# Kernel tuning notes

Hardware: AMD Instinct MI355X
Metric: run time of the kernel (lower is better)

The kernel has to match this reference:

```python
import jax, jax.numpy as jnp
import numpy as np

N_MELS = 20
NUM_FRAMES = 32
FRAME_LEN = 512
SR = NUM_FRAMES * FRAME_LEN  # 16384
EPS = np.finfo(np.float64).eps  # matches np.finfo(float).eps in original


def _mel_filters(n_fft, sr, n_mels, fmin, fmax):
    """Replicates librosa.filters.mel(..., htk=False, norm=None) in pure numpy."""
    f_sp = 200.0 / 3.0
    min_log_hz = 1000.0
    min_log_mel = min_log_hz / f_sp
    logstep = np.log(6.4) / 27.0

    def hz_to_mel(f):
        f = np.asarray(f, dtype=np.float64)
        return np.where(f >= min_log_hz,
                        min_log_mel + np.log(np.maximum(f, 1e-10) / min_log_hz) / logstep,
                        f / f_sp)

    def mel_to_hz(m):
        m = np.asarray(m, dtype=np.float64)
        return np.where(m >= min_log_mel,
                        min_log_hz * np.exp(logstep * (m - min_log_mel)),
                        f_sp * m)

    fftfreqs = np.linspace(0.0, sr / 2.0, 1 + n_fft // 2)
    mels = np.linspace(hz_to_mel(fmin), hz_to_mel(fmax), n_mels + 2)
    mel_f = mel_to_hz(mels)
    fdiff = np.diff(mel_f)
    ramps = mel_f[:, None] - fftfreqs[None, :]
    lower = -ramps[:-2] / fdiff[:-1, None]
    upper = ramps[2:] / fdiff[1:, None]
    weights = np.maximum(0.0, np.minimum(lower, upper))  # norm=None -> no scaling
    return weights.astype(np.float32)  # (n_mels, 1+n_fft//2)


def setup_inputs() -> dict:
    key = jax.random.key(0)
    inputs = jax.random.normal(key, (4096, NUM_FRAMES, FRAME_LEN), dtype=jnp.float32)
    filter_banks = jnp.asarray(_mel_filters(FRAME_LEN, SR, N_MELS, 0.0, SR / 2.0 + 1.0))
    hw = jnp.asarray(np.hamming(FRAME_LEN).astype(np.float32))
    return {"inputs": inputs, "filter_banks": filter_banks, "hw": hw}


def reference(inputs, filter_banks, hw):
    # Hamming window + forward-normalized rFFT; original squares only the REAL part.
    fft_real = jnp.fft.rfft(inputs * hw, norm="forward").real  # (B, 32, 257)
    mag = fft_real * fft_real
    mels = jnp.einsum("mf,btf->btm", filter_banks, mag)  # (B, 32, 20)
    mels = jnp.where(mels == 0, jnp.float32(EPS), mels)
    log_mels = jnp.log2(mels)
    return jnp.floor(log_mels)[..., None]  # (B, 32, 20, 1)
```

## Files before the change

kernel.cpp:

```cpp
#include <hip/hip_runtime.h>
#include <math.h>


#define MARGIN_L2 1.0e-3f
#define IDX(e) ((e) + ((e) >> 3))
#define WCSTRIDE 20

__device__ __forceinline__ float4 f4add(float4 a, float4 b) {
    return make_float4(a.x + b.x, a.y + b.y, a.z + b.z, a.w + b.w);
}
__device__ __forceinline__ float4 f4sub(float4 a, float4 b) {
    return make_float4(a.x - b.x, a.y - b.y, a.z - b.z, a.w - b.w);
}
__device__ __forceinline__ float4 cmulc4(float2 w, float4 z) {
    return make_float4(w.x * z.x + w.y * z.y, w.x * z.y - w.y * z.x,
                       w.x * z.z + w.y * z.w, w.x * z.w - w.y * z.z);
}

__device__ __forceinline__ void bfly4(int s, int l, float2 w1, float2 w2,
                                      float4 x1, float4 y1, float4 x2, float4 y2,
                                      float4* dst) {
    const int j = l >> s;
    const int r = l & ((1 << s) - 1);
    const float4 u1 = f4add(x1, y1);
    const float4 v1 = cmulc4(w1, f4sub(x1, y1));
    const float4 u2 = f4add(x2, y2);
    const float4 m  = cmulc4(w1, f4sub(x2, y2));
    const float4 v2 = make_float4(m.y, -m.x, m.w, -m.z);
    const float4 o0 = f4add(u1, u2);
    const float4 o1 = cmulc4(w2, f4sub(u1, u2));
    const float4 o2 = f4add(v1, v2);
    const float4 o3 = cmulc4(w2, f4sub(v1, v2));
    const int eb = (j << (s + 2)) + r;
    dst[IDX(eb)]            = o0;
    dst[IDX(eb + (1 << s))] = o2;
    dst[IDX(eb + (2 << s))] = o1;
    dst[IDX(eb + (3 << s))] = o3;
}

__device__ __forceinline__ void load_stage0(
    const float* __restrict__ x, int f0, int f1, int l,
    float2 h0, float2 h1, float2 h2, float2 h3,
    float2 w1, float2 w2, float4* W)
{
    const float2* xa = (const float2*)(x + (size_t)f0 * 512);
    const float2* xb = (const float2*)(x + (size_t)f1 * 512);
    const float2 a0 = xa[l],       a1 = xa[l + 64];
    const float2 a2 = xa[l + 128], a3 = xa[l + 192];
    const float2 b0 = xb[l],       b1 = xb[l + 64];
    const float2 b2 = xb[l + 128], b3 = xb[l + 192];
    const float4 x1 = make_float4(a0.x * h0.x, a0.y * h0.y,
                                  b0.x * h0.x, b0.y * h0.y);
    const float4 x2 = make_float4(a1.x * h1.x, a1.y * h1.y,
                                  b1.x * h1.x, b1.y * h1.y);
    const float4 y1 = make_float4(a2.x * h2.x, a2.y * h2.y,
                                  b2.x * h2.x, b2.y * h2.y);
    const float4 y2 = make_float4(a3.x * h3.x, a3.y * h3.y,
                                  b3.x * h3.x, b3.y * h3.y);
    bfly4(0, l, w1, w2, x1, y1, x2, y2, W);
}

__global__ void prep_full(const float* __restrict__ fb,
                          double* __restrict__ tw64,
                          float4* __restrict__ twp,
                          float4* __restrict__ wc,
                          int*    __restrict__ meta,
                          unsigned* count) {
    __shared__ float2 s_tw[256];
    __shared__ int sg0[20], sng[20];
    const int t = threadIdx.x;
    double s, c;
    sincospi((double)t * (1.0 / 256.0), &s, &c);
    tw64[t]       = c;
    tw64[256 + t] = s;
    s_tw[t] = make_float2((float)c, (float)s);

    if (t < 20) {
        int lo = 257, hi = 0;
        for (int k = 0; k < 257; k++) {
            if (fb[t * 257 + k] > 0.0f) {
                if (k < lo) lo = k;
                hi = k + 1;
            }
        }
        if (hi <= lo) { lo = 0; hi = 1; }
        int g0 = lo >> 2;
        int ng = ((hi + 3) >> 2) - g0;
        if (ng > WCSTRIDE) ng = WCSTRIDE;
        sg0[t] = g0; sng[t] = ng;
        meta[t] = g0 | (ng << 16);
    }
    __syncthreads();

    if (t < 64) {
        const float2 a0 = s_tw[2 * t],        b0 = s_tw[4 * t];
        twp[t]        = make_float4(a0.x, a0.y, b0.x, b0.y);
        const float2 a2 = s_tw[8 * (t >> 2)], b2 = s_tw[16 * (t >> 2)];
        twp[64 + t]   = make_float4(a2.x, a2.y, b2.x, b2.y);
        const float2 a4 = s_tw[32 * (t >> 4)], b4 = s_tw[64 * (t >> 4)];
        twp[128 + t]  = make_float4(a4.x, a4.y, b4.x, b4.y);
        const float2 u0 = s_tw[t],            u1 = s_tw[t + 64];
        twp[192 + t]  = make_float4(u0.x, u0.y, u1.x, u1.y);
    }

    for (int i = t; i < 20 * WCSTRIDE; i += 256) {
        const int m = i / WCSTRIDE, j = i % WCSTRIDE;
        float4 v = make_float4(0.0f, 0.0f, 0.0f, 0.0f);
        if (j < sng[m]) {
            const int b = (sg0[m] + j) * 4;
            const float* row = fb + m * 257;
            v.x = (b + 0 < 257) ? row[b + 0] : 0.0f;
            v.y = (b + 1 < 257) ? row[b + 1] : 0.0f;
            v.z = (b + 2 < 257) ? row[b + 2] : 0.0f;
            v.w = (b + 3 < 257) ? row[b + 3] : 0.0f;
        }
        wc[i] = v;
    }
    if (count && t == 0) *count = 0;
}

__global__ void prep_tw64(double* __restrict__ tw64) {
    const int t = threadIdx.x;
    double s, c;
    sincospi((double)t * (1.0 / 256.0), &s, &c);
    tw64[t]       = c;
    tw64[256 + t] = s;
}

__global__ __launch_bounds__(256, 4) void phase1(
    const float* __restrict__ x,
    const float* __restrict__ hw,
    const float4* __restrict__ twp,
    const float4* __restrict__ wc,
    const int*    __restrict__ meta,
    float* __restrict__ out,
    unsigned* __restrict__ count,
    unsigned* __restrict__ worklist)
{
    __shared__ __align__(16) float4 buf[8][288];

    const int t = threadIdx.x;
    const int w = t >> 6;
    const int l = t & 63;
    const int base = (blockIdx.x * 4 + w) * 4;
    const int fg0 = base, fg1 = base + 1, fg2 = base + 2, fg3 = base + 3;

    const float4 tp0 = twp[l];
    const float4 tp2 = twp[64 + l];
    const float4 tp4 = twp[128 + l];
    const float4 tpU = twp[192 + l];
    const float2 w0s = make_float2(tp0.x, tp0.y), w0d = make_float2(tp0.z, tp0.w);
    const float2 w2s = make_float2(tp2.x, tp2.y), w2d = make_float2(tp2.z, tp2.w);
    const float2 w4s = make_float2(tp4.x, tp4.y), w4d = make_float2(tp4.z, tp4.w);

    float4* const WA = &buf[2 * w][0];
    float4* const WB = &buf[2 * w + 1][0];

    const float2* hp = (const float2*)hw;
    const float2 h0 = hp[l],       h1 = hp[l + 64];
    const float2 h2 = hp[l + 128], h3 = hp[l + 192];

    load_stage0(x, fg0, fg1, l, h0, h1, h2, h3, w0s, w0d, WA);
    load_stage0(x, fg2, fg3, l, h0, h1, h2, h3, w0s, w0d, WB);
    __builtin_amdgcn_wave_barrier();

    {
        const float4 ax1 = WA[IDX(l)],      ay1 = WA[IDX(l + 128)];
        const float4 ax2 = WA[IDX(l + 64)], ay2 = WA[IDX(l + 192)];
        const float4 bx1 = WB[IDX(l)],      by1 = WB[IDX(l + 128)];
        const float4 bx2 = WB[IDX(l + 64)], by2 = WB[IDX(l + 192)];
        bfly4(2, l, w2s, w2d, ax1, ay1, ax2, ay2, WA);
        bfly4(2, l, w2s, w2d, bx1, by1, bx2, by2, WB);
        __builtin_amdgcn_wave_barrier();
    }
    {
        const float4 ax1 = WA[IDX(l)],      ay1 = WA[IDX(l + 128)];
        const float4 ax2 = WA[IDX(l + 64)], ay2 = WA[IDX(l + 192)];
        const float4 bx1 = WB[IDX(l)],      by1 = WB[IDX(l + 128)];
        const float4 bx2 = WB[IDX(l + 64)], by2 = WB[IDX(l + 192)];
        bfly4(4, l, w4s, w4d, ax1, ay1, ax2, ay2, WA);
        bfly4(4, l, w4s, w4d, bx1, by1, bx2, by2, WB);
        __builtin_amdgcn_wave_barrier();
    }
    {
        const float4 ax1 = WA[IDX(l)],      ay1 = WA[IDX(l + 128)];
        const float4 ax2 = WA[IDX(l + 64)], ay2 = WA[IDX(l + 192)];
        const float4 bx1 = WB[IDX(l)],      by1 = WB[IDX(l + 128)];
        const float4 bx2 = WB[IDX(l + 64)], by2 = WB[IDX(l + 192)];
        {
            const float4 u1 = f4add(ax1, ay1);
            const float4 v1 = f4sub(ax1, ay1);
            const float4 u2 = f4add(ax2, ay2);
            const float4 m  = f4sub(ax2, ay2);
            const float4 v2 = make_float4(m.y, -m.x, m.w, -m.z);
            WA[IDX(l)]       = f4add(u1, u2);
            WA[IDX(l + 64)]  = f4add(v1, v2);
            WA[IDX(l + 128)] = f4sub(u1, u2);
            WA[IDX(l + 192)] = f4sub(v1, v2);
        }
        {
            const float4 u1 = f4add(bx1, by1);
            const float4 v1 = f4sub(bx1, by1);
            const float4 u2 = f4add(bx2, by2);
            const float4 m  = f4sub(bx2, by2);
            const float4 v2 = make_float4(m.y, -m.x, m.w, -m.z);
            WB[IDX(l)]       = f4add(u1, u2);
            WB[IDX(l + 64)]  = f4add(v1, v2);
            WB[IDX(l + 128)] = f4sub(u1, u2);
            WB[IDX(l + 192)] = f4sub(v1, v2);
        }
    }
    __builtin_amdgcn_wave_barrier();

    float2* const pwrA = (float2*)WA;
    float2* const pwrB = (float2*)WB;
    {
        const float4 zk0A = WA[IDX(l)];
        const float4 zc0A = WA[IDX((256 - l) & 255)];
        const float4 zk1A = WA[IDX(l + 64)];
        const float4 zc1A = WA[IDX(192 - l)];
        const float4 zmA  = WA[IDX(128)];
        const float4 zk0B = WB[IDX(l)];
        const float4 zc0B = WB[IDX((256 - l) & 255)];
        const float4 zk1B = WB[IDX(l + 64)];
        const float4 zc1B = WB[IDX(192 - l)];
        const float4 zmB  = WB[IDX(128)];
        const float2 u0 = make_float2(tpU.x, tpU.y);
        const float2 u1 = make_float2(tpU.z, tpU.w);
        __builtin_amdgcn_wave_barrier();

#define UNTANGLE_PAIR(zk, zc, wk, p, kk, kc)                                 \
        {                                                                    \
            const float Sr0 = zk.x + zc.x, Si0 = zk.y + zc.y;                \
            const float Dr0 = zk.x - zc.x;                                   \
            const float Sr1 = zk.z + zc.z, Si1 = zk.w + zc.w;                \
            const float Dr1 = zk.z - zc.z;                                   \
            const float E0 = 0.5f * Sr0;                                     \
            const float T0 = 0.5f * (wk.x * Si0 - wk.y * Dr0);               \
            const float E1 = 0.5f * Sr1;                                     \
            const float T1 = 0.5f * (wk.x * Si1 - wk.y * Dr1);               \
            const float a0 = (E0 + T0) * (1.0f / 512.0f);                    \
            const float a1 = (E1 + T1) * (1.0f / 512.0f);                    \
            const float b0 = (E0 - T0) * (1.0f / 512.0f);                    \
            const float b1 = (E1 - T1) * (1.0f / 512.0f);                    \
            p[kk] = make_float2(a0 * a0, a1 * a1);                           \
            p[kc] = make_float2(b0 * b0, b1 * b1);                           \
        }
        UNTANGLE_PAIR(zk0A, zc0A, u0, pwrA, l, 256 - l)
        UNTANGLE_PAIR(zk1A, zc1A, u1, pwrA, l + 64, 192 - l)
        UNTANGLE_PAIR(zk0B, zc0B, u0, pwrB, l, 256 - l)
        UNTANGLE_PAIR(zk1B, zc1B, u1, pwrB, l + 64, 192 - l)
#undef UNTANGLE_PAIR
        if (l == 0) {
            const float vA0 = zmA.x * (1.0f / 512.0f);
            const float vA1 = zmA.z * (1.0f / 512.0f);
            pwrA[128] = make_float2(vA0 * vA0, vA1 * vA1);
            const float vB0 = zmB.x * (1.0f / 512.0f);
            const float vB1 = zmB.z * (1.0f / 512.0f);
            pwrB[128] = make_float2(vB0 * vB0, vB1 * vB1);
        }
        if (l >= 57) {
            pwrA[257 + (l - 57)] = make_float2(0.0f, 0.0f);
            pwrB[257 + (l - 57)] = make_float2(0.0f, 0.0f);
        }
    }
    __builtin_amdgcn_wave_barrier();

    float aA = 0.0f, aB = 0.0f, aC = 0.0f, aD = 0.0f;
    if (l < 60) {
        const int mel = l % 20;
        const int sub = l / 20;
        const int mw  = meta[mel];
        const int g0m = mw & 0xffff;
        const int ngm = mw >> 16;
        const float4* wrow = wc + mel * WCSTRIDE;
        const float4* pwA4 = (const float4*)pwrA + 2 * g0m;
        const float4* pwB4 = (const float4*)pwrB + 2 * g0m;
        for (int j = sub; j < ngm; j += 3) {
            const float4 w4  = wrow[j];
            const float4 qa0 = pwA4[2 * j];
            const float4 qa1 = pwA4[2 * j + 1];
            const float4 qb0 = pwB4[2 * j];
            const float4 qb1 = pwB4[2 * j + 1];
            aA = fmaf(w4.w, qa1.z, fmaf(w4.z, qa1.x,
                 fmaf(w4.y, qa0.z, fmaf(w4.x, qa0.x, aA))));
            aB = fmaf(w4.w, qa1.w, fmaf(w4.z, qa1.y,
                 fmaf(w4.y, qa0.w, fmaf(w4.x, qa0.y, aB))));
            aC = fmaf(w4.w, qb1.z, fmaf(w4.z, qb1.x,
                 fmaf(w4.y, qb0.z, fmaf(w4.x, qb0.x, aC))));
            aD = fmaf(w4.w, qb1.w, fmaf(w4.z, qb1.y,
                 fmaf(w4.y, qb0.w, fmaf(w4.x, qb0.y, aD))));
        }
    }
    const float pA1 = __shfl(aA, l + 20), pA2 = __shfl(aA, l + 40);
    const float pB1 = __shfl(aB, l + 20), pB2 = __shfl(aB, l + 40);
    const float pC1 = __shfl(aC, l + 20), pC2 = __shfl(aC, l + 40);
    const float pD1 = __shfl(aD, l + 20), pD2 = __shfl(aD, l + 40);

    int fl0 = 0, fl1 = 0, fl2 = 0, fl3 = 0;
    if (l < 20) {
#define FINISH(acc, p1, p2, fg, flag)                                        \
        {                                                                    \
            const float v = acc + p1 + p2;                                   \
            float fl;                                                        \
            if (v < 1e-30f) { fl = -52.0f; flag = 1; }                       \
            else {                                                           \
                const float l2 = log2f(v);                                   \
                fl = floorf(l2);                                             \
                flag = (l2 - fl < MARGIN_L2) | ((fl + 1.0f - l2) < MARGIN_L2);\
            }                                                                \
            out[(size_t)fg * 20 + l] = fl;                                   \
        }
        FINISH(aA, pA1, pA2, fg0, fl0)
        FINISH(aB, pB1, pB2, fg1, fl1)
        FINISH(aC, pC1, pC2, fg2, fl2)
        FINISH(aD, pD1, pD2, fg3, fl3)
#undef FINISH
    }
    const unsigned long long b0 = __ballot(fl0);
    const unsigned long long b1 = __ballot(fl1);
    const unsigned long long b2 = __ballot(fl2);
    const unsigned long long b3 = __ballot(fl3);
    if (l == 0) {
        const unsigned nf = (b0 != 0ULL) + (b1 != 0ULL)
                          + (b2 != 0ULL) + (b3 != 0ULL);
        if (nf) {
            unsigned idx = atomicAdd(count, nf);
            if (b0 != 0ULL) worklist[idx++] = (unsigned)fg0;
            if (b1 != 0ULL) worklist[idx++] = (unsigned)fg1;
            if (b2 != 0ULL) worklist[idx++] = (unsigned)fg2;
            if (b3 != 0ULL) worklist[idx]   = (unsigned)fg3;
        }
    }
}

__global__ __launch_bounds__(256) void phase2_wl(
    const float* __restrict__ x,
    const float* __restrict__ fb,
    const float* __restrict__ hw,
    const double* __restrict__ tw64,
    const unsigned* __restrict__ count,
    const unsigned* __restrict__ worklist,
    float* __restrict__ out)
{
    __shared__ double Are[256], Aim[256], Bre[256], Bim[256];
    __shared__ double ltc[256], lts[256];
    __shared__ double pwr[257];

    const int t = threadIdx.x;
    ltc[t] = tw64[t];
    lts[t] = tw64[256 + t];
    __syncthreads();

    const unsigned n = *count;
    for (unsigned i = blockIdx.x; i < n; i += gridDim.x) {
        const int f = (int)worklist[i];

        {
            const float2 xv = ((const float2*)x)[(size_t)f * 256 + t];
            const float2 hv = ((const float2*)hw)[t];
            Are[t] = (double)xv.x * (double)hv.x;
            Aim[t] = (double)xv.y * (double)hv.y;
        }
        __syncthreads();

        double* sre = Are; double* sim = Aim;
        double* dre = Bre; double* dim = Bim;
        const int p = t & 127;
        const int which = t >> 7;
#pragma unroll
        for (int s = 0; s < 8; s++) {
            const int j = p >> s;
            const double ar = sre[p],       ai = sim[p];
            const double br = sre[p + 128], bi = sim[p + 128];
            double orr, oi;
            int dpos;
            if (which) {
                const int idx = j << (s + 1);
                const double wr = ltc[idx];
                const double wi = -lts[idx];
                const double ur = ar - br, ui = ai - bi;
                orr = wr * ur - wi * ui;
                oi  = wr * ui + wi * ur;
                dpos = p + ((j + 1) << s);
            } else {
                orr = ar + br;
                oi  = ai + bi;
                dpos = p + (j << s);
            }
            dre[dpos] = orr;
            dim[dpos] = oi;
            __syncthreads();
            double* tmp;
            tmp = sre; sre = dre; dre = tmp;
            tmp = sim; sim = dim; dim = tmp;
        }

        {
            const double a = sre[t], b = sim[t];
            const int t2 = (256 - t) & 255;
            const double c = sre[t2], d = sim[t2];
            const double rex = 0.5 * (a + c)
                             + 0.5 * (ltc[t] * (b + d) - lts[t] * (a - c));
            const double v = rex * (1.0 / 512.0);
            pwr[t] = v * v;
            if (t == 0) {
                const double vn = (a - b) * (1.0 / 512.0);
                pwr[256] = vn * vn;
            }
        }
        __syncthreads();

        if (t < 160) {
            const int mel = t >> 3;
            const int sub = t & 7;
            const float* wrow = fb + mel * 257;
            double acc = 0.0;
            for (int k = sub; k < 257; k += 8)
                acc = fma((double)wrow[k], pwr[k], acc);
            acc += __shfl_down(acc, 4, 8);
            acc += __shfl_down(acc, 2, 8);
            acc += __shfl_down(acc, 1, 8);
            if (sub == 0) {
                double v = acc;
                if (v == 0.0) v = 2.220446049250313e-16;
                out[(size_t)f * 20 + mel] = (float)floor(log2(v));
            }
        }
        __syncthreads();
    }
}

__global__ __launch_bounds__(256) void f64_all(
    const float*  __restrict__ x,
    const float*  __restrict__ fb,
    const float*  __restrict__ hw,
    const double* __restrict__ tw,
    float* __restrict__ out)
{
    __shared__ double Are[256], Aim[256], Bre[256], Bim[256];
    __shared__ double ltc[256], lts[256];
    __shared__ double pwr[257];

    const int t = threadIdx.x;
    const int f = blockIdx.x;

    ltc[t] = tw[t];
    lts[t] = tw[256 + t];
    {
        const float2 xv = ((const float2*)x)[(size_t)f * 256 + t];
        const float2 hv = ((const float2*)hw)[t];
        Are[t] = (double)xv.x * (double)hv.x;
        Aim[t] = (double)xv.y * (double)hv.y;
    }
    __syncthreads();

    double* sre = Are; double* sim = Aim;
    double* dre = Bre; double* dim = Bim;
    const int p = t & 127;
    const int which = t >> 7;
#pragma unroll
    for (int s = 0; s < 8; s++) {
        const int j = p >> s;
        const double ar = sre[p],       ai = sim[p];
        const double br = sre[p + 128], bi = sim[p + 128];
        double orr, oi;
        int dpos;
        if (which) {
            const int idx = j << (s + 1);
            const double wr = ltc[idx];
            const double wi = -lts[idx];
            const double ur = ar - br, ui = ai - bi;
            orr = wr * ur - wi * ui;
            oi  = wr * ui + wi * ur;
            dpos = p + ((j + 1) << s);
        } else {
            orr = ar + br;
            oi  = ai + bi;
            dpos = p + (j << s);
        }
        dre[dpos] = orr;
        dim[dpos] = oi;
        __syncthreads();
        double* tmp;
        tmp = sre; sre = dre; dre = tmp;
        tmp = sim; sim = dim; dim = tmp;
    }

    {
        const double a = sre[t], b = sim[t];
        const int t2 = (256 - t) & 255;
        const double c = sre[t2], d = sim[t2];
        const double rex = 0.5 * (a + c)
                         + 0.5 * (ltc[t] * (b + d) - lts[t] * (a - c));
        const double v = rex * (1.0 / 512.0);
        pwr[t] = v * v;
        if (t == 0) {
            const double vn = (a - b) * (1.0 / 512.0);
            pwr[256] = vn * vn;
        }
    }
    __syncthreads();

    if (t < 160) {
        const int mel = t >> 3;
        const int sub = t & 7;
        const float* wrow = fb + mel * 257;
        double acc = 0.0;
        for (int k = sub; k < 257; k += 8)
            acc = fma((double)wrow[k], pwr[k], acc);
        acc += __shfl_down(acc, 4, 8);
        acc += __shfl_down(acc, 2, 8);
        acc += __shfl_down(acc, 1, 8);
        if (sub == 0) {
            double v = acc;
            if (v == 0.0) v = 2.220446049250313e-16;
            out[(size_t)f * 20 + mel] = (float)floor(log2(v));
        }
    }
}

extern "C" void kernel_launch(void* const* d_in, const int* in_sizes, int n_in,
                              void* d_out, int out_size, void* d_ws, size_t ws_size,
                              hipStream_t stream) {
    const float* x  = (const float*)d_in[0];
    const float* fb = (const float*)d_in[1];
    const float* hw = (const float*)d_in[2];
    float* out = (float*)d_out;

    const int frames = in_sizes[0] / 512;

    char* ws = (char*)d_ws;
    double* tw64 = (double*)ws;
    float4* twp  = (float4*)(ws + 4096);
    float4* wc   = (float4*)(ws + 8192);
    int*    meta = (int*)(ws + 14592);

    const size_t T1 = 32832 + 4 * (size_t)frames;

    if (ws_size >= T1 && (frames % 16) == 0) {
        unsigned* count    = (unsigned*)(ws + 32768);
        unsigned* worklist = (unsigned*)(ws + 32832);
        prep_full<<<1, 256, 0, stream>>>(fb, tw64, twp, wc, meta, count);
        phase1<<<frames / 16, 256, 0, stream>>>(x, hw, twp, wc, meta, out,
                                                count, worklist);
        phase2_wl<<<4096, 256, 0, stream>>>(x, fb, hw, tw64, count, worklist, out);
    } else {
        prep_tw64<<<1, 256, 0, stream>>>(tw64);
        f64_all<<<frames, 256, 0, stream>>>(x, fb, hw, tw64, out);
    }
}
```

Baseline: 415.9 us.

## Rewrite fp64 fallback pass as one-frame-per-wave radix-4 FFT with banded mel weights

The fp64 recompute kernel for flagged frames now assigns one frame to each wavefront instead of each block. It uses a radix-4 FFT in double2 shared memory with wave-level barriers in place of block-wide syncs, plus precomputed double twiddles. The mel projection uses the banded compact weight table rather than all 257 bins. prep_full also parallelizes the filter-band extent scan across threads. This trims sync and arithmetic overhead in phase2, at the cost of more shared memory per block and extra prep work.

```diff
diff --git a/kernel.cpp b/kernel.cpp
--- a/kernel.cpp
+++ b/kernel.cpp
@@ -15,6 +15,15 @@
 __device__ __forceinline__ float4 cmulc4(float2 w, float4 z) {
     return make_float4(w.x * z.x + w.y * z.y, w.x * z.y - w.y * z.x,
                        w.x * z.z + w.y * z.w, w.x * z.w - w.y * z.z);
+}
+__device__ __forceinline__ double2 d2add(double2 a, double2 b) {
+    return make_double2(a.x + b.x, a.y + b.y);
+}
+__device__ __forceinline__ double2 d2sub(double2 a, double2 b) {
+    return make_double2(a.x - b.x, a.y - b.y);
+}
+__device__ __forceinline__ double2 cmulcd(double2 w, double2 z) {
+    return make_double2(w.x * z.x + w.y * z.y, w.x * z.y - w.y * z.x);
 }
 
 __device__ __forceinline__ void bfly4(int s, int l, float2 w1, float2 w2,
@@ -31,6 +40,27 @@
     const float4 o1 = cmulc4(w2, f4sub(u1, u2));
     const float4 o2 = f4add(v1, v2);
     const float4 o3 = cmulc4(w2, f4sub(v1, v2));
+    const int eb = (j << (s + 2)) + r;
+    dst[IDX(eb)]            = o0;
+    dst[IDX(eb + (1 << s))] = o2;
+    dst[IDX(eb + (2 << s))] = o1;
+    dst[IDX(eb + (3 << s))] = o3;
+}
+
+__device__ __forceinline__ void bfly4d(int s, int l, double2 w1, double2 w2,
+                                       double2 x1, double2 y1, double2 x2,
+                                       double2 y2, double2* dst) {
+    const int j = l >> s;
+    const int r = l & ((1 << s) - 1);
+    const double2 u1 = d2add(x1, y1);
+    const double2 v1 = cmulcd(w1, d2sub(x1, y1));
+    const double2 u2 = d2add(x2, y2);
+    const double2 m  = cmulcd(w1, d2sub(x2, y2));
+    const double2 v2 = make_double2(m.y, -m.x);
+    const double2 o0 = d2add(u1, u2);
+    const double2 o1 = cmulcd(w2, d2sub(u1, u2));
+    const double2 o2 = d2add(v1, v2);
+    const double2 o3 = cmulcd(w2, d2sub(v1, v2));
     const int eb = (j << (s + 2)) + r;
     dst[IDX(eb)]            = o0;
     dst[IDX(eb + (1 << s))] = o2;
@@ -63,26 +93,36 @@
 __global__ void prep_full(const float* __restrict__ fb,
                           double* __restrict__ tw64,
                           float4* __restrict__ twp,
+                          double4* __restrict__ twq,
                           float4* __restrict__ wc,
                           int*    __restrict__ meta,
                           unsigned* count) {
     __shared__ float2 s_tw[256];
-    __shared__ int sg0[20], sng[20];
+    __shared__ double sc[256], ss[256];
+    __shared__ int slo[20], shi[20], sg0[20], sng[20];
     const int t = threadIdx.x;
     double s, c;
     sincospi((double)t * (1.0 / 256.0), &s, &c);
     tw64[t]       = c;
     tw64[256 + t] = s;
+    sc[t] = c; ss[t] = s;
     s_tw[t] = make_float2((float)c, (float)s);
+    if (t < 20) { slo[t] = 257; shi[t] = 0; }
+    __syncthreads();
+
+    if (t < 240) {
+        const int m = t / 12, part = t % 12;
+        const int k0 = part * 22;
+        int k1 = k0 + 22; if (k1 > 257) k1 = 257;
+        int lo = 257, hi = 0;
+        for (int k = k0; k < k1; k++)
+            if (fb[m * 257 + k] > 0.0f) { if (k < lo) lo = k; hi = k + 1; }
+        if (hi > lo) { atomicMin(&slo[m], lo); atomicMax(&shi[m], hi); }
+    }
+    __syncthreads();
 
     if (t < 20) {
-        int lo = 257, hi = 0;
-        for (int k = 0; k < 257; k++) {
-            if (fb[t * 257 + k] > 0.0f) {
-                if (k < lo) lo = k;
-                hi = k + 1;
-            }
-        }
+        int lo = slo[t], hi = shi[t];
         if (hi <= lo) { lo = 0; hi = 1; }
         int g0 = lo >> 2;
         int ng = ((hi + 3) >> 2) - g0;
@@ -90,8 +130,6 @@
         sg0[t] = g0; sng[t] = ng;
         meta[t] = g0 | (ng << 16);
     }
-    __syncthreads();
-
     if (t < 64) {
         const float2 a0 = s_tw[2 * t],        b0 = s_tw[4 * t];
         twp[t]        = make_float4(a0.x, a0.y, b0.x, b0.y);
@@ -101,7 +139,14 @@
         twp[128 + t]  = make_float4(a4.x, a4.y, b4.x, b4.y);
         const float2 u0 = s_tw[t],            u1 = s_tw[t + 64];
         twp[192 + t]  = make_float4(u0.x, u0.y, u1.x, u1.y);
-    }
+        twq[t]       = make_double4(sc[2*t], ss[2*t], sc[4*t], ss[4*t]);
+        twq[64 + t]  = make_double4(sc[8*(t>>2)],  ss[8*(t>>2)],
+                                    sc[16*(t>>2)], ss[16*(t>>2)]);
+        twq[128 + t] = make_double4(sc[32*(t>>4)], ss[32*(t>>4)],
+                                    sc[64*(t>>4)], ss[64*(t>>4)]);
+        twq[192 + t] = make_double4(sc[t], ss[t], sc[t+64], ss[t+64]);
+    }
+    __syncthreads();
 
     for (int i = t; i < 20 * WCSTRIDE; i += 256) {
         const int m = i / WCSTRIDE, j = i % WCSTRIDE;
@@ -334,100 +379,140 @@
     }
 }
 
-__global__ __launch_bounds__(256) void phase2_wl(
+__global__ __launch_bounds__(256, 4) void phase2_wl(
     const float* __restrict__ x,
-    const float* __restrict__ fb,
     const float* __restrict__ hw,
-    const double* __restrict__ tw64,
+    const double4* __restrict__ twq,
+    const float4* __restrict__ wc,
+    const int*    __restrict__ meta,
     const unsigned* __restrict__ count,
     const unsigned* __restrict__ worklist,
     float* __restrict__ out)
 {
-    __shared__ double Are[256], Aim[256], Bre[256], Bim[256];
-    __shared__ double ltc[256], lts[256];
-    __shared__ double pwr[257];
+    __shared__ __align__(16) double2 dbuf[4][288];
 
     const int t = threadIdx.x;
-    ltc[t] = tw64[t];
-    lts[t] = tw64[256 + t];
-    __syncthreads();
+    const int w = t >> 6;
+    const int l = t & 63;
+    double2* const W = &dbuf[w][0];
+    double* const pwr = (double*)W;
 
     const unsigned n = *count;
-    for (unsigned i = blockIdx.x; i < n; i += gridDim.x) {
+    const unsigned stride = gridDim.x * 4;
+    for (unsigned i = blockIdx.x * 4 + (unsigned)w; i < n; i += stride) {
         const int f = (int)worklist[i];
 
         {
-            const float2 xv = ((const float2*)x)[(size_t)f * 256 + t];
-            const float2 hv = ((const float2*)hw)[t];
-            Are[t] = (double)xv.x * (double)hv.x;
-            Aim[t] = (double)xv.y * (double)hv.y;
-        }
-        __syncthreads();
-
-        double* sre = Are; double* sim = Aim;
-        double* dre = Bre; double* dim = Bim;
-        const int p = t & 127;
-        const int which = t >> 7;
-#pragma unroll
-        for (int s = 0; s < 8; s++) {
-            const int j = p >> s;
-            const double ar = sre[p],       ai = sim[p];
-            const double br = sre[p + 128], bi = sim[p + 128];
-            double orr, oi;
-            int dpos;
-            if (which) {
-                const int idx = j << (s + 1);
-                const double wr = ltc[idx];
-                const double wi = -lts[idx];
-                const double ur = ar - br, ui = ai - bi;
-                orr = wr * ur - wi * ui;
-                oi  = wr * ui + wi * ur;
-                dpos = p + ((j + 1) << s);
-            } else {
-                orr = ar + br;
-                oi  = ai + bi;
-                dpos = p + (j << s);
+            const double4 tq = twq[l];
+            const float2* xa = (const float2*)(x + (size_t)f * 512);
+            const float2* hp = (const float2*)hw;
+            const float2 a0 = xa[l],       a1 = xa[l + 64];
+            const float2 a2 = xa[l + 128], a3 = xa[l + 192];
+            const float2 h0 = hp[l],       h1 = hp[l + 64];
+            const float2 h2 = hp[l + 128], h3 = hp[l + 192];
+            const double2 x1 = make_double2((double)a0.x * (double)h0.x,
+                                            (double)a0.y * (double)h0.y);
+            const double2 x2 = make_double2((double)a1.x * (double)h1.x,
+                                            (double)a1.y * (double)h1.y);
+            const double2 y1 = make_double2((double)a2.x * (double)h2.x,
+                                            (double)a2.y * (double)h2.y);
+            const double2 y2 = make_double2((double)a3.x * (double)h3.x,
+                                            (double)a3.y * (double)h3.y);
+            bfly4d(0, l, make_double2(tq.x, tq.y), make_double2(tq.z, tq.w),
+                   x1, y1, x2, y2, W);
+        }
+        __builtin_amdgcn_wave_barrier();
+        {
+            const double4 tq = twq[64 + l];
+            const double2 x1 = W[IDX(l)],      y1 = W[IDX(l + 128)];
+            const double2 x2 = W[IDX(l + 64)], y2 = W[IDX(l + 192)];
+            bfly4d(2, l, make_double2(tq.x, tq.y), make_double2(tq.z, tq.w),
+                   x1, y1, x2, y2, W);
+        }
+        __builtin_amdgcn_wave_barrier();
+        {
+            const double4 tq = twq[128 + l];
+            const double2 x1 = W[IDX(l)],      y1 = W[IDX(l + 128)];
+            const double2 x2 = W[IDX(l + 64)], y2 = W[IDX(l + 192)];
+            bfly4d(4, l, make_double2(tq.x, tq.y), make_double2(tq.z, tq.w),
+                   x1, y1, x2, y2, W);
+        }
+        __builtin_amdgcn_wave_barrier();
+        {
+            const double2 x1 = W[IDX(l)],      y1 = W[IDX(l + 128)];
+            const double2 x2 = W[IDX(l + 64)], y2 = W[IDX(l + 192)];
+            const double2 u1 = d2add(x1, y1);
+            const double2 v1 = d2sub(x1, y1);
+            const double2 u2 = d2add(x2, y2);
+            const double2 m  = d2sub(x2, y2);
+            const double2 v2 = make_double2(m.y, -m.x);
+            W[IDX(l)]       = d2add(u1, u2);
+            W[IDX(l + 64)]  = d2add(v1, v2);
+            W[IDX(l + 128)] = d2sub(u1, u2);
+            W[IDX(l + 192)] = d2sub(v1, v2);
+        }
+        __builtin_amdgcn_wave_barrier();
+        {
+            const double4 tq = twq[192 + l];
+            const double2 zk0 = W[IDX(l)];
+            const double2 zc0 = W[IDX((256 - l) & 255)];
+            const double2 zk1 = W[IDX(l + 64)];
+            const double2 zc1 = W[IDX(192 - l)];
+            const double2 zm  = W[IDX(128)];
+            __builtin_amdgcn_wave_barrier();
+            {
+                const double Sr = zk0.x + zc0.x, Si = zk0.y + zc0.y;
+                const double Dr = zk0.x - zc0.x;
+                const double E = 0.5 * Sr, T = 0.5 * (tq.x * Si - tq.y * Dr);
+                const double a = (E + T) * (1.0 / 512.0);
+                const double b = (E - T) * (1.0 / 512.0);
+                pwr[l]       = a * a;
+                pwr[256 - l] = b * b;
             }
-            dre[dpos] = orr;
-            dim[dpos] = oi;
-            __syncthreads();
-            double* tmp;
-            tmp = sre; sre = dre; dre = tmp;
-            tmp = sim; sim = dim; dim = tmp;
-        }
-
-        {
-            const double a = sre[t], b = sim[t];
-            const int t2 = (256 - t) & 255;
-            const double c = sre[t2], d = sim[t2];
-            const double rex = 0.5 * (a + c)
-                             + 0.5 * (ltc[t] * (b + d) - lts[t] * (a - c));
-            const double v = rex * (1.0 / 512.0);
-            pwr[t] = v * v;
-            if (t == 0) {
-                const double vn = (a - b) * (1.0 / 512.0);
-                pwr[256] = vn * vn;
+            {
+                const double Sr = zk1.x + zc1.x, Si = zk1.y + zc1.y;
+                const double Dr = zk1.x - zc1.x;
+                const double E = 0.5 * Sr, T = 0.5 * (tq.z * Si - tq.w * Dr);
+                const double a = (E + T) * (1.0 / 512.0);
+                const double b = (E - T) * (1.0 / 512.0);
+                pwr[l + 64]  = a * a;
+                pwr[192 - l] = b * b;
             }
-        }
-        __syncthreads();
-
-        if (t < 160) {
-            const int mel = t >> 3;
-            const int sub = t & 7;
-            const float* wrow = fb + mel * 257;
-            double acc = 0.0;
-            for (int k = sub; k < 257; k += 8)
-                acc = fma((double)wrow[k], pwr[k], acc);
-            acc += __shfl_down(acc, 4, 8);
-            acc += __shfl_down(acc, 2, 8);
-            acc += __shfl_down(acc, 1, 8);
-            if (sub == 0) {
-                double v = acc;
-                if (v == 0.0) v = 2.220446049250313e-16;
-                out[(size_t)f * 20 + mel] = (float)floor(log2(v));
+            if (l == 0) {
+                const double v = zm.x * (1.0 / 512.0);
+                pwr[128] = v * v;
             }
-        }
-        __syncthreads();
+            if (l < 3) pwr[257 + l] = 0.0;
+        }
+        __builtin_amdgcn_wave_barrier();
+
+        double acc = 0.0;
+        if (l < 60) {
+            const int mel = l % 20;
+            const int sub = l / 20;
+            const int mw  = meta[mel];
+            const int g0m = mw & 0xffff;
+            const int ngm = mw >> 16;
+            const float4* wrow = wc + mel * WCSTRIDE;
+            const double2* pw2 = (const double2*)pwr + 2 * g0m;
+            for (int j = sub; j < ngm; j += 3) {
+                const float4 w4 = wrow[j];
+                const double2 q0 = pw2[2 * j];
+                const double2 q1 = pw2[2 * j + 1];
+                acc = fma((double)w4.x, q0.x, acc);
+                acc = fma((double)w4.y, q0.y, acc);
+                acc = fma((double)w4.z, q1.x, acc);
+                acc = fma((double)w4.w, q1.y, acc);
+            }
+        }
+        const double p1 = __shfl(acc, l + 20);
+        const double p2 = __shfl(acc, l + 40);
+        if (l < 20) {
+            double v = acc + p1 + p2;
+            if (v == 0.0) v = 2.220446049250313e-16;
+            out[(size_t)f * 20 + l] = (float)floor(log2(v));
+        }
+        __builtin_amdgcn_wave_barrier();
     }
 }
 
@@ -531,20 +616,22 @@
     const int frames = in_sizes[0] / 512;
 
     char* ws = (char*)d_ws;
-    double* tw64 = (double*)ws;
-    float4* twp  = (float4*)(ws + 4096);
-    float4* wc   = (float4*)(ws + 8192);
-    int*    meta = (int*)(ws + 14592);
+    double*  tw64 = (double*)ws;
+    float4*  twp  = (float4*)(ws + 4096);
+    float4*  wc   = (float4*)(ws + 8192);
+    int*     meta = (int*)(ws + 14592);
+    double4* twq  = (double4*)(ws + 16384);
 
     const size_t T1 = 32832 + 4 * (size_t)frames;
 
     if (ws_size >= T1 && (frames % 16) == 0) {
         unsigned* count    = (unsigned*)(ws + 32768);
         unsigned* worklist = (unsigned*)(ws + 32832);
-        prep_full<<<1, 256, 0, stream>>>(fb, tw64, twp, wc, meta, count);
+        prep_full<<<1, 256, 0, stream>>>(fb, tw64, twp, twq, wc, meta, count);
         phase1<<<frames / 16, 256, 0, stream>>>(x, hw, twp, wc, meta, out,
                                                 count, worklist);
-        phase2_wl<<<4096, 256, 0, stream>>>(x, fb, hw, tw64, count, worklist, out);
+        phase2_wl<<<2048, 256, 0, stream>>>(x, hw, twq, wc, meta,
+                                            count, worklist, out);
     } else {
         prep_tw64<<<1, 256, 0, stream>>>(tw64);
         f64_all<<<frames, 256, 0, stream>>>(x, fb, hw, tw64, out);
```

Result: faster. 378.5 us (-9.0%).
